# Kernel optimization log

Measured on AMD Instinct MI355X. Metric: run time of the kernel, lower is better.

## Reference

```python
import jax, jax.numpy as jnp
import numpy as np

B, C_IN, T_IN = 128, 128, 2500
C_OUT, K, STRIDE, PAD = 64, 27, 4, 13  # T_out = 625
BN_EPS = 1e-5
SURROGATE_ALPHA = 4.0


def binarize_weight(w):
    """1-bit (XNOR-Net style) weight quantization with straight-through estimator.
    w: (O, I, K). Per-output-channel scale = mean |w|."""
    alpha = jnp.mean(jnp.abs(w), axis=(1, 2), keepdims=True)
    wq = jnp.sign(w) * alpha
    return w + jax.lax.stop_gradient(wq - w)


def spike(x):
    """Heaviside spike with sigmoid surrogate gradient (STE)."""
    hard = (x > 0).astype(x.dtype)
    soft = jax.nn.sigmoid(SURROGATE_ALPHA * x)
    return soft + jax.lax.stop_gradient(hard - soft)


def setup_inputs() -> dict:
    key = jax.random.key(0)
    ks = jax.random.split(key, 8)
    scale_conv = 1.0 / np.sqrt(C_IN * K)
    scale_lin = 1.0 / np.sqrt(C_OUT)
    return {
        "x": jax.random.normal(ks[0], (B, C_IN, T_IN), dtype=jnp.float32),
        "conv_w": jax.random.normal(ks[1], (C_OUT, C_IN, K), dtype=jnp.float32) * scale_conv,
        "conv_b": jnp.zeros((C_OUT,), dtype=jnp.float32),
        "bn_gamma": jnp.ones((C_OUT,), dtype=jnp.float32),
        "bn_beta": jnp.zeros((C_OUT,), dtype=jnp.float32),
        "bn_mean": jax.random.normal(ks[2], (C_OUT,), dtype=jnp.float32) * 0.1,
        "bn_var": jax.random.uniform(ks[3], (C_OUT,), dtype=jnp.float32, minval=0.5, maxval=1.5),
        "wq": jax.random.normal(ks[4], (C_OUT, C_OUT), dtype=jnp.float32) * scale_lin,
        "wk": jax.random.normal(ks[5], (C_OUT, C_OUT), dtype=jnp.float32) * scale_lin,
        "wv": jax.random.normal(ks[6], (C_OUT, C_OUT), dtype=jnp.float32) * scale_lin,
        "wo": jax.random.normal(ks[7], (C_OUT, C_OUT), dtype=jnp.float32) * scale_lin,
    }


def reference(x, conv_w, conv_b, bn_gamma, bn_beta, bn_mean, bn_var, wq, wk, wv, wo):
    # --- 1-bit quantized conv1d, stride 4 ---
    w_bin = binarize_weight(conv_w)
    y = jax.lax.conv_general_dilated(
        x, w_bin, window_strides=(STRIDE,), padding=[(PAD, PAD)],
        dimension_numbers=("NCH", "OIH", "NCH"))
    y = y + conv_b[None, :, None]  # (B, C_OUT, 625)

    # --- BatchNorm1d (inference stats) + ELU ---
    inv = jax.lax.rsqrt(bn_var + BN_EPS)
    y = (y - bn_mean[None, :, None]) * (inv * bn_gamma)[None, :, None] + bn_beta[None, :, None]
    y = jax.nn.elu(y)

    # --- Global spiking attention (single head) ---
    s = spike(y)                                   # (B, C, T) binary spikes
    q = jnp.einsum("oc,bct->bot", wq, s)           # (B, C, T)
    k = jnp.einsum("oc,bct->bot", wk, s)
    v = jnp.einsum("oc,bct->bot", wv, y)
    scores = jnp.einsum("bct,bcs->bts", q, k) / jnp.sqrt(jnp.asarray(C_OUT, y.dtype))
    attn = jax.nn.softmax(scores, axis=-1)         # (B, T, T)
    ctx = jnp.einsum("bts,bcs->bct", attn, v)      # (B, C, T)
    out = y + jnp.einsum("oc,bct->bot", wo, ctx)   # residual
    return out
```

## Files before the change

kernel.cpp:

```cpp
#include <hip/hip_runtime.h>
#include <math.h>

#define B_    128
#define CIN   128
#define TIN   2500
#define COUT  64
#define KW    27
#define TOUT  625
#define TPAD  640
#define CTT   32
#define GROWS 152

typedef __bf16 bf16x8 __attribute__((ext_vector_type(8)));
typedef float  f32x4  __attribute__((ext_vector_type(4)));

__device__ __forceinline__ unsigned short f32_to_bf16_rne(float v) {
    unsigned u = __float_as_uint(v);
    u += 0x7FFFu + ((u >> 16) & 1u);
    return (unsigned short)(u >> 16);
}

__device__ __forceinline__ f32x4 mfma_bf16(bf16x8 a, bf16x8 b, f32x4 c) {
    return __builtin_amdgcn_mfma_f32_16x16x32_bf16(a, b, c, 0, 0, 0);
}

__device__ __forceinline__ bf16x8 expand_sgn(unsigned b) {
    union { unsigned u[4]; bf16x8 v; } r;
#pragma unroll
    for (int j = 0; j < 4; j++) {
        unsigned lo = (b >> (2 * j)) & 1u;
        unsigned hi = (b >> (2 * j + 1)) & 1u;
        r.u[j] = 0x3F803F80u | (lo << 15) | (hi << 31);
    }
    return r.v;
}

__global__ void binarize_kernel(const float* __restrict__ w,
                                unsigned* __restrict__ sgn2,
                                float* __restrict__ alpha_out) {
    int o = blockIdx.x, tid = threadIdx.x;
    __shared__ float red[256];
    const float* wo_ = w + (size_t)o * (CIN * KW);
    float s = 0.f;
    for (int idx = tid; idx < CIN * KW; idx += 256) s += fabsf(wo_[idx]);
    red[tid] = s;
    __syncthreads();
    for (int st = 128; st > 0; st >>= 1) {
        if (tid < st) red[tid] += red[tid + st];
        __syncthreads();
    }
    if (tid == 0) alpha_out[o] = red[0] / (float)(CIN * KW);

    for (int t = tid; t < KW * 4; t += 256) {
        int kk = t >> 2, kg = t & 3;
        unsigned u = 0;
#pragma unroll
        for (int cs = 0; cs < 4; cs++) {
#pragma unroll
            for (int j = 0; j < 8; j++) {
                int c = cs * 32 + kg * 8 + j;
                float v = wo_[c * KW + kk];
                unsigned bit = (v > 0.f) ? 0u : 1u;
                u |= bit << (cs * 8 + j);
            }
        }
        sgn2[(kk * 4 + kg) * 64 + o] = u;
    }
}

__global__ void transpose_w_kernel(const float* __restrict__ wq, const float* __restrict__ wk,
                                   const float* __restrict__ wv, const float* __restrict__ wo,
                                   const float* __restrict__ conv_b, const float* __restrict__ gamma_,
                                   const float* __restrict__ beta_, const float* __restrict__ mean_,
                                   const float* __restrict__ var_, const float* __restrict__ alpha_,
                                   float* __restrict__ dstT,
                                   unsigned short* __restrict__ wo_h, unsigned short* __restrict__ wo_l,
                                   float* __restrict__ scA, float* __restrict__ scB) {
    if (blockIdx.x < 3) {
        const float* srcs[3] = {wq, wk, wv};
        const float* src = srcs[blockIdx.x];
        float* dst = dstT + (size_t)blockIdx.x * 4096;
        for (int idx = threadIdx.x; idx < 4096; idx += 256) {
            int o = idx >> 6, c = idx & 63;
            dst[c * 64 + o] = src[idx];
        }
    } else if (blockIdx.x == 3) {
        for (int idx = threadIdx.x; idx < 4096; idx += 256) {
            float v = wo[idx];
            unsigned short h = f32_to_bf16_rne(v);
            float hf = __uint_as_float((unsigned)h << 16);
            wo_h[idx] = h;
            wo_l[idx] = f32_to_bf16_rne(v - hf);
        }
    } else {
        int o = threadIdx.x;
        if (o < 64) {
            float inv = rsqrtf(var_[o] + 1e-5f);
            float G = gamma_[o] * inv;
            scA[o] = alpha_[o] * G;
            scB[o] = (conv_b[o] - mean_[o]) * G + beta_[o];
        }
    }
}

__global__ __launch_bounds__(256, 4) void conv_kernel(
    const float* __restrict__ x, const unsigned* __restrict__ sgn2,
    const float* __restrict__ scA, const float* __restrict__ scB,
    float* __restrict__ y_out)
{
    __shared__ __align__(16) unsigned short xhi[GROWS * 128];

    int b = blockIdx.y;
    int t0 = blockIdx.x * CTT;
    int tid = threadIdx.x;

    const float* xb = x + (size_t)b * CIN * TIN;
    int gbase = 4 * t0 - 13;
    for (int task = tid; task < 16 * GROWS; task += 256) {
        int c8 = task / GROWS, gl = task - c8 * GROWS;
        int g = gbase + gl;
        bool valid = (gl < 151) && ((unsigned)g < (unsigned)TIN);
        float vs[8];
#pragma unroll
        for (int j = 0; j < 8; j++)
            vs[j] = valid ? xb[(size_t)(c8 * 8 + j) * TIN + g] : 0.f;
        union { unsigned u[4]; uint4 q; } H;
#pragma unroll
        for (int j = 0; j < 4; j++) {
            unsigned short h0 = f32_to_bf16_rne(vs[2 * j]);
            unsigned short h1 = f32_to_bf16_rne(vs[2 * j + 1]);
            H.u[j] = (unsigned)h0 | ((unsigned)h1 << 16);
        }
        int c8p = c8 ^ ((gl >> 2) & 15);
        *(uint4*)(xhi + gl * 128 + c8p * 8) = H.q;
    }
    __syncthreads();

    int wave = tid >> 6, lane = tid & 63;
    int o0 = wave * 16;
    int n = lane & 15, kg = lane >> 4;

    f32x4 acc0 = {0.f, 0.f, 0.f, 0.f};
    f32x4 acc1 = {0.f, 0.f, 0.f, 0.f};

    const unsigned* sgb = sgn2 + (size_t)kg * 64 + o0 + n;
    unsigned sa = sgb[0];

#pragma unroll 1
    for (int kk = 0; kk < KW; ++kk) {
        unsigned na = 0;
        if (kk < KW - 1) na = sgb[(kk + 1) * 256];
        int gl = 4 * n + kk;
        int rot = (gl >> 2) & 15;
        const unsigned short* xr0 = xhi + gl * 128;
        const unsigned short* xr1 = xr0 + 8192;
#pragma unroll
        for (int cs = 0; cs < 4; ++cs) {
            int c8p = (cs * 4 + kg) ^ rot;
            bf16x8 b0 = *(const bf16x8*)(xr0 + c8p * 8);
            bf16x8 b1 = *(const bf16x8*)(xr1 + c8p * 8);
            bf16x8 a = expand_sgn((sa >> (8 * cs)) & 0xFFu);
            acc0 = mfma_bf16(a, b0, acc0);
            acc1 = mfma_bf16(a, b1, acc1);
        }
        sa = na;
    }

    int quad = lane >> 4, col = lane & 15;
#pragma unroll
    for (int tt = 0; tt < 2; ++tt) {
        int t_g = t0 + tt * 16 + col;
        if (t_g < TOUT) {
            f32x4 a = tt ? acc1 : acc0;
#pragma unroll
            for (int r = 0; r < 4; ++r) {
                int o = o0 + quad * 4 + r;
                float s = a[r] * scA[o] + scB[o];
                float yv = s > 0.f ? s : expm1f(s);
                y_out[((size_t)b * COUT + o) * TOUT + t_g] = yv;
            }
        }
    }
}

__global__ __launch_bounds__(256, 2) void proj_kernel(
    const float* __restrict__ y, const float* __restrict__ wqT,
    const float* __restrict__ wkT, const float* __restrict__ wvT,
    unsigned short* __restrict__ q_h, unsigned short* __restrict__ k_h,
    unsigned short* __restrict__ vT_h)
{
    __shared__ float y_sh[64 * 132];
    int b = blockIdx.y, t0 = blockIdx.x * 128, tid = threadIdx.x;

    const float* yb = y + (size_t)b * COUT * TOUT;
    for (int i = tid; i < 64 * 128; i += 256) {
        int c = i >> 7, tt = i & 127;
        int t = t0 + tt;
        y_sh[c * 132 + tt] = (t < TOUT) ? yb[c * TOUT + t] : 0.f;
    }
    __syncthreads();

    int oo = tid & 63, tq = tid >> 6;
    float q[32], k[32], v[32];
#pragma unroll
    for (int j = 0; j < 32; j++) { q[j] = 0.f; k[j] = 0.f; v[j] = 0.f; }

#pragma unroll 1
    for (int c = 0; c < 64; ++c) {
        float wq = wqT[c * 64 + oo];
        float wk = wkT[c * 64 + oo];
        float wv = wvT[c * 64 + oo];
        const float* yr = &y_sh[c * 132 + tq * 32];
#pragma unroll
        for (int j = 0; j < 32; ++j) {
            float yv = yr[j];
            float sp = yv > 0.f ? 1.f : 0.f;
            q[j] += wq * sp; k[j] += wk * sp; v[j] += wv * yv;
        }
    }

    int tbase = t0 + tq * 32;
#pragma unroll
    for (int j = 0; j < 32; ++j) {
        size_t off = ((size_t)b * TPAD + tbase + j) * 64 + oo;
        q_h[off] = f32_to_bf16_rne(q[j]);
        k_h[off] = f32_to_bf16_rne(k[j]);
    }
    union { unsigned short u[32]; uint4 q4[4]; } V;
#pragma unroll
    for (int j = 0; j < 32; ++j) V.u[j] = f32_to_bf16_rne(v[j]);
    unsigned short* vp = vT_h + ((size_t)b * 64 + oo) * TPAD + tbase;
#pragma unroll
    for (int i = 0; i < 4; i++) ((uint4*)vp)[i] = V.q4[i];
}

__global__ __launch_bounds__(256, 3) void attn_kernel(
    const unsigned short* __restrict__ q_h, const unsigned short* __restrict__ k_h,
    const unsigned short* __restrict__ vT_h, const float* __restrict__ y,
    const unsigned short* __restrict__ wo_h, const unsigned short* __restrict__ wo_l,
    float* __restrict__ out)
{
    __shared__ float sc_sh[16 * 648];
    __shared__ float ctx_sh[64 * 17];
    __shared__ float red_sh[256];
    __shared__ float rden[16];

    int b = blockIdx.y, t0 = blockIdx.x * 16, tid = threadIdx.x;
    int wave = tid >> 6, lane = tid & 63;
    int quad = lane >> 4, nlo = lane & 15;

    const unsigned short* qb = q_h + ((size_t)b * TPAD + t0 + nlo) * 64 + quad * 8;
    bf16x8 qa0 = *(const bf16x8*)(qb);
    bf16x8 qa1 = *(const bf16x8*)(qb + 32);
    const unsigned short* kbase = k_h + (size_t)b * TPAD * 64 + quad * 8;
#pragma unroll 5
    for (int nt = 0; nt < 10; ++nt) {
        int s = (wave * 10 + nt) * 16 + nlo;
        const unsigned short* krow = kbase + (size_t)s * 64;
        bf16x8 kb0 = *(const bf16x8*)(krow);
        bf16x8 kb1 = *(const bf16x8*)(krow + 32);
        f32x4 acc = {0.f, 0.f, 0.f, 0.f};
        acc = mfma_bf16(qa0, kb0, acc);
        acc = mfma_bf16(qa1, kb1, acc);
#pragma unroll
        for (int r = 0; r < 4; ++r)
            sc_sh[(quad * 4 + r) * 648 + s] = acc[r] * 0.125f;
    }
    __syncthreads();

    int ti1 = tid >> 4, sg = tid & 15;
    float mx = -3.0e38f;
    for (int s = sg; s < TOUT; s += 16) mx = fmaxf(mx, sc_sh[ti1 * 648 + s]);
    red_sh[tid] = mx;
    __syncthreads();
    float rowm = red_sh[ti1 * 16];
#pragma unroll
    for (int l = 1; l < 16; l++) rowm = fmaxf(rowm, red_sh[ti1 * 16 + l]);
    __syncthreads();
    float sum = 0.f;
    for (int s = sg; s < TOUT; s += 16) {
        float e = __expf(sc_sh[ti1 * 648 + s] - rowm);
        sc_sh[ti1 * 648 + s] = e;
        sum += e;
    }
    red_sh[tid] = sum;
    __syncthreads();
    if (tid < 16) {
        float tot = 0.f;
#pragma unroll
        for (int l = 0; l < 16; l++) tot += red_sh[tid * 16 + l];
        rden[tid] = 1.f / tot;
    }
    __syncthreads();

    const unsigned short* vb = vT_h + ((size_t)b * 64 + wave * 16 + nlo) * TPAD;
    f32x4 cacc = {0.f, 0.f, 0.f, 0.f};
#pragma unroll 4
    for (int ks = 0; ks < 20; ++ks) {
        const float* pr = &sc_sh[nlo * 648 + ks * 32 + quad * 8];
        union { unsigned short u[8]; bf16x8 v; } P;
#pragma unroll
        for (int j = 0; j < 8; ++j) P.u[j] = f32_to_bf16_rne(pr[j]);
        bf16x8 v8 = *(const bf16x8*)(vb + ks * 32 + quad * 8);
        cacc = mfma_bf16(P.v, v8, cacc);
    }
#pragma unroll
    for (int r = 0; r < 4; ++r)
        ctx_sh[(wave * 16 + nlo) * 17 + quad * 4 + r] = cacc[r] * rden[quad * 4 + r];
    __syncthreads();

    const unsigned short* woh = wo_h + (size_t)(wave * 16 + nlo) * 64 + quad * 8;
    const unsigned short* wol = wo_l + (size_t)(wave * 16 + nlo) * 64 + quad * 8;
    f32x4 oacc = {0.f, 0.f, 0.f, 0.f};
#pragma unroll
    for (int ks = 0; ks < 2; ++ks) {
        union { unsigned short u[8]; bf16x8 v; } Bc;
#pragma unroll
        for (int j = 0; j < 8; ++j)
            Bc.u[j] = f32_to_bf16_rne(ctx_sh[(ks * 32 + quad * 8 + j) * 17 + nlo]);
        bf16x8 ah = *(const bf16x8*)(woh + ks * 32);
        bf16x8 al = *(const bf16x8*)(wol + ks * 32);
        oacc = mfma_bf16(ah, Bc.v, oacc);
        oacc = mfma_bf16(al, Bc.v, oacc);
    }
    int t_g = t0 + nlo;
    if (t_g < TOUT) {
#pragma unroll
        for (int r = 0; r < 4; ++r) {
            int o = wave * 16 + quad * 4 + r;
            size_t off = ((size_t)b * COUT + o) * TOUT + t_g;
            out[off] = y[off] + oacc[r];
        }
    }
}

extern "C" void kernel_launch(void* const* d_in, const int* in_sizes, int n_in,
                              void* d_out, int out_size, void* d_ws, size_t ws_size,
                              hipStream_t stream) {
    const float* x        = (const float*)d_in[0];
    const float* conv_w   = (const float*)d_in[1];
    const float* conv_b   = (const float*)d_in[2];
    const float* bn_gamma = (const float*)d_in[3];
    const float* bn_beta  = (const float*)d_in[4];
    const float* bn_mean  = (const float*)d_in[5];
    const float* bn_var   = (const float*)d_in[6];
    const float* wq       = (const float*)d_in[7];
    const float* wk       = (const float*)d_in[8];
    const float* wv       = (const float*)d_in[9];
    const float* wo       = (const float*)d_in[10];
    float* out = (float*)d_out;
    float* ws  = (float*)d_ws;

    unsigned* sgn2        = (unsigned*)ws;
    float* alpha          = ws + 110592;
    float* scA            = ws + 110656;
    float* scB            = ws + 110720;
    float* wT4            = ws + 110848;
    unsigned short* wo_h  = (unsigned short*)(ws + 123136);
    unsigned short* wo_l  = (unsigned short*)(ws + 125184);
    float* yb             = ws + 131072;
    unsigned short* q_h   = (unsigned short*)(ws + 5251072);
    unsigned short* k_h   = (unsigned short*)(ws + 7872512);
    unsigned short* vT_h  = (unsigned short*)(ws + 10493952);

    hipLaunchKernelGGL(binarize_kernel, dim3(64), dim3(256), 0, stream, conv_w, sgn2, alpha);
    hipLaunchKernelGGL(transpose_w_kernel, dim3(5), dim3(256), 0, stream,
                       wq, wk, wv, wo, conv_b, bn_gamma, bn_beta, bn_mean, bn_var, alpha,
                       wT4, wo_h, wo_l, scA, scB);
    hipLaunchKernelGGL(conv_kernel, dim3(20, 128), dim3(256), 0, stream,
                       x, sgn2, scA, scB, yb);
    hipLaunchKernelGGL(proj_kernel, dim3(5, 128), dim3(256), 0, stream,
                       yb, wT4, wT4 + 4096, wT4 + 8192, q_h, k_h, vT_h);
    hipLaunchKernelGGL(attn_kernel, dim3(40, 128), dim3(256), 0, stream,
                       q_h, k_h, vT_h, yb, wo_h, wo_l, out);
}
```

Before: 497.8 us.

## Double attention block width and halve proj tile with shared-memory weights

The attention kernel now runs 512 threads per block. The score, softmax and P·V stages are split across 8 waves, and the two K-halves of the context are reduced through shared memory before the output projection, which only 4 waves perform. The projection kernel uses 64-wide time tiles, which doubles the grid and cuts per-thread accumulators from 96 to 48. It also stages Wq/Wk/Wv into shared memory and reads y as float4. The aim is more parallelism and occupancy on the 128x40 attention grid and lower register pressure in the projection. The cost is more synchronisation, idle waves during the output projection, and more shared memory per block.

```diff
diff --git a/kernel.cpp b/kernel.cpp
--- a/kernel.cpp
+++ b/kernel.cpp
@@ -189,60 +189,73 @@
     unsigned short* __restrict__ q_h, unsigned short* __restrict__ k_h,
     unsigned short* __restrict__ vT_h)
 {
-    __shared__ float y_sh[64 * 132];
-    int b = blockIdx.y, t0 = blockIdx.x * 128, tid = threadIdx.x;
-
+    __shared__ float w_sh[3 * 4096];
+    __shared__ __align__(16) float y_sh[64 * 72];
+    int b = blockIdx.y, t0 = blockIdx.x * 64, tid = threadIdx.x;
+
+    for (int i = tid; i < 4096; i += 256) {
+        w_sh[i]         = wqT[i];
+        w_sh[4096 + i]  = wkT[i];
+        w_sh[8192 + i]  = wvT[i];
+    }
     const float* yb = y + (size_t)b * COUT * TOUT;
-    for (int i = tid; i < 64 * 128; i += 256) {
-        int c = i >> 7, tt = i & 127;
+    for (int i = tid; i < 64 * 64; i += 256) {
+        int c = i >> 6, tt = i & 63;
         int t = t0 + tt;
-        y_sh[c * 132 + tt] = (t < TOUT) ? yb[c * TOUT + t] : 0.f;
+        y_sh[c * 72 + tt] = (t < TOUT) ? yb[c * TOUT + t] : 0.f;
     }
     __syncthreads();
 
     int oo = tid & 63, tq = tid >> 6;
-    float q[32], k[32], v[32];
-#pragma unroll
-    for (int j = 0; j < 32; j++) { q[j] = 0.f; k[j] = 0.f; v[j] = 0.f; }
+    float q[16], k[16], v[16];
+#pragma unroll
+    for (int j = 0; j < 16; j++) { q[j] = 0.f; k[j] = 0.f; v[j] = 0.f; }
 
 #pragma unroll 1
     for (int c = 0; c < 64; ++c) {
-        float wq = wqT[c * 64 + oo];
-        float wk = wkT[c * 64 + oo];
-        float wv = wvT[c * 64 + oo];
-        const float* yr = &y_sh[c * 132 + tq * 32];
-#pragma unroll
-        for (int j = 0; j < 32; ++j) {
-            float yv = yr[j];
-            float sp = yv > 0.f ? 1.f : 0.f;
-            q[j] += wq * sp; k[j] += wk * sp; v[j] += wv * yv;
-        }
-    }
-
-    int tbase = t0 + tq * 32;
-#pragma unroll
-    for (int j = 0; j < 32; ++j) {
+        float wq = w_sh[c * 64 + oo];
+        float wk = w_sh[4096 + c * 64 + oo];
+        float wv = w_sh[8192 + c * 64 + oo];
+        const float* yr = &y_sh[c * 72 + tq * 16];
+#pragma unroll
+        for (int j4 = 0; j4 < 4; ++j4) {
+            float4 y4 = *(const float4*)(yr + 4 * j4);
+            float ys[4] = {y4.x, y4.y, y4.z, y4.w};
+#pragma unroll
+            for (int j = 0; j < 4; ++j) {
+                float yv = ys[j];
+                float sp = yv > 0.f ? 1.f : 0.f;
+                q[4 * j4 + j] += wq * sp;
+                k[4 * j4 + j] += wk * sp;
+                v[4 * j4 + j] += wv * yv;
+            }
+        }
+    }
+
+    int tbase = t0 + tq * 16;
+#pragma unroll
+    for (int j = 0; j < 16; ++j) {
         size_t off = ((size_t)b * TPAD + tbase + j) * 64 + oo;
         q_h[off] = f32_to_bf16_rne(q[j]);
         k_h[off] = f32_to_bf16_rne(k[j]);
     }
-    union { unsigned short u[32]; uint4 q4[4]; } V;
-#pragma unroll
-    for (int j = 0; j < 32; ++j) V.u[j] = f32_to_bf16_rne(v[j]);
+    union { unsigned short u[16]; uint4 q4[2]; } V;
+#pragma unroll
+    for (int j = 0; j < 16; ++j) V.u[j] = f32_to_bf16_rne(v[j]);
     unsigned short* vp = vT_h + ((size_t)b * 64 + oo) * TPAD + tbase;
-#pragma unroll
-    for (int i = 0; i < 4; i++) ((uint4*)vp)[i] = V.q4[i];
-}
-
-__global__ __launch_bounds__(256, 3) void attn_kernel(
+    ((uint4*)vp)[0] = V.q4[0];
+    ((uint4*)vp)[1] = V.q4[1];
+}
+
+__global__ __launch_bounds__(512, 3) void attn_kernel(
     const unsigned short* __restrict__ q_h, const unsigned short* __restrict__ k_h,
     const unsigned short* __restrict__ vT_h, const float* __restrict__ y,
     const unsigned short* __restrict__ wo_h, const unsigned short* __restrict__ wo_l,
     float* __restrict__ out)
 {
     __shared__ float sc_sh[16 * 648];
-    __shared__ float ctx_sh[64 * 17];
-    __shared__ float red_sh[256];
+    __shared__ float ctx_sh[2 * 64 * 17];
+    __shared__ float red_sh[512];
     __shared__ float rden[16];
 
     int b = blockIdx.y, t0 = blockIdx.x * 16, tid = threadIdx.x;
@@ -254,8 +267,8 @@
     bf16x8 qa1 = *(const bf16x8*)(qb + 32);
     const unsigned short* kbase = k_h + (size_t)b * TPAD * 64 + quad * 8;
 #pragma unroll 5
-    for (int nt = 0; nt < 10; ++nt) {
-        int s = (wave * 10 + nt) * 16 + nlo;
+    for (int nt = 0; nt < 5; ++nt) {
+        int s = wave * 80 + nt * 16 + nlo;
         const unsigned short* krow = kbase + (size_t)s * 64;
         bf16x8 kb0 = *(const bf16x8*)(krow);
         bf16x8 kb1 = *(const bf16x8*)(krow + 32);
@@ -268,17 +281,17 @@
     }
     __syncthreads();
 
-    int ti1 = tid >> 4, sg = tid & 15;
+    int ti1 = tid >> 5, sg = tid & 31;
     float mx = -3.0e38f;
-    for (int s = sg; s < TOUT; s += 16) mx = fmaxf(mx, sc_sh[ti1 * 648 + s]);
+    for (int s = sg; s < TOUT; s += 32) mx = fmaxf(mx, sc_sh[ti1 * 648 + s]);
     red_sh[tid] = mx;
     __syncthreads();
-    float rowm = red_sh[ti1 * 16];
-#pragma unroll
-    for (int l = 1; l < 16; l++) rowm = fmaxf(rowm, red_sh[ti1 * 16 + l]);
+    float rowm = red_sh[ti1 * 32];
+#pragma unroll
+    for (int l = 1; l < 32; l++) rowm = fmaxf(rowm, red_sh[ti1 * 32 + l]);
     __syncthreads();
     float sum = 0.f;
-    for (int s = sg; s < TOUT; s += 16) {
+    for (int s = sg; s < TOUT; s += 32) {
         float e = __expf(sc_sh[ti1 * 648 + s] - rowm);
         sc_sh[ti1 * 648 + s] = e;
         sum += e;
@@ -288,15 +301,18 @@
     if (tid < 16) {
         float tot = 0.f;
 #pragma unroll
-        for (int l = 0; l < 16; l++) tot += red_sh[tid * 16 + l];
+        for (int l = 0; l < 32; l++) tot += red_sh[tid * 32 + l];
         rden[tid] = 1.f / tot;
     }
     __syncthreads();
 
-    const unsigned short* vb = vT_h + ((size_t)b * 64 + wave * 16 + nlo) * TPAD;
+    int cw = (wave & 3) * 16, kh = wave >> 2;
+    const unsigned short* vb = vT_h + ((size_t)b * 64 + cw + nlo) * TPAD;
     f32x4 cacc = {0.f, 0.f, 0.f, 0.f};
-#pragma unroll 4
-    for (int ks = 0; ks < 20; ++ks) {
+    int ks0 = kh * 10;
+#pragma unroll 5
+    for (int i = 0; i < 10; ++i) {
+        int ks = ks0 + i;
         const float* pr = &sc_sh[nlo * 648 + ks * 32 + quad * 8];
         union { unsigned short u[8]; bf16x8 v; } P;
 #pragma unroll
@@ -306,30 +322,35 @@
     }
 #pragma unroll
     for (int r = 0; r < 4; ++r)
-        ctx_sh[(wave * 16 + nlo) * 17 + quad * 4 + r] = cacc[r] * rden[quad * 4 + r];
-    __syncthreads();
-
-    const unsigned short* woh = wo_h + (size_t)(wave * 16 + nlo) * 64 + quad * 8;
-    const unsigned short* wol = wo_l + (size_t)(wave * 16 + nlo) * 64 + quad * 8;
-    f32x4 oacc = {0.f, 0.f, 0.f, 0.f};
-#pragma unroll
-    for (int ks = 0; ks < 2; ++ks) {
-        union { unsigned short u[8]; bf16x8 v; } Bc;
-#pragma unroll
-        for (int j = 0; j < 8; ++j)
-            Bc.u[j] = f32_to_bf16_rne(ctx_sh[(ks * 32 + quad * 8 + j) * 17 + nlo]);
-        bf16x8 ah = *(const bf16x8*)(woh + ks * 32);
-        bf16x8 al = *(const bf16x8*)(wol + ks * 32);
-        oacc = mfma_bf16(ah, Bc.v, oacc);
-        oacc = mfma_bf16(al, Bc.v, oacc);
-    }
-    int t_g = t0 + nlo;
-    if (t_g < TOUT) {
-#pragma unroll
-        for (int r = 0; r < 4; ++r) {
-            int o = wave * 16 + quad * 4 + r;
-            size_t off = ((size_t)b * COUT + o) * TOUT + t_g;
-            out[off] = y[off] + oacc[r];
+        ctx_sh[kh * 1088 + (cw + nlo) * 17 + quad * 4 + r] = cacc[r] * rden[quad * 4 + r];
+    __syncthreads();
+
+    if (wave < 4) {
+        const unsigned short* woh = wo_h + (size_t)(wave * 16 + nlo) * 64 + quad * 8;
+        const unsigned short* wol = wo_l + (size_t)(wave * 16 + nlo) * 64 + quad * 8;
+        f32x4 oacc = {0.f, 0.f, 0.f, 0.f};
+#pragma unroll
+        for (int ks = 0; ks < 2; ++ks) {
+            union { unsigned short u[8]; bf16x8 v; } Bc;
+#pragma unroll
+            for (int j = 0; j < 8; ++j) {
+                int c = ks * 32 + quad * 8 + j;
+                float cv = ctx_sh[c * 17 + nlo] + ctx_sh[1088 + c * 17 + nlo];
+                Bc.u[j] = f32_to_bf16_rne(cv);
+            }
+            bf16x8 ah = *(const bf16x8*)(woh + ks * 32);
+            bf16x8 al = *(const bf16x8*)(wol + ks * 32);
+            oacc = mfma_bf16(ah, Bc.v, oacc);
+            oacc = mfma_bf16(al, Bc.v, oacc);
+        }
+        int t_g = t0 + nlo;
+        if (t_g < TOUT) {
+#pragma unroll
+            for (int r = 0; r < 4; ++r) {
+                int o = wave * 16 + quad * 4 + r;
+                size_t off = ((size_t)b * COUT + o) * TOUT + t_g;
+                out[off] = y[off] + oacc[r];
+            }
         }
     }
 }
@@ -369,8 +390,8 @@
                        wT4, wo_h, wo_l, scA, scB);
     hipLaunchKernelGGL(conv_kernel, dim3(20, 128), dim3(256), 0, stream,
                        x, sgn2, scA, scB, yb);
-    hipLaunchKernelGGL(proj_kernel, dim3(5, 128), dim3(256), 0, stream,
+    hipLaunchKernelGGL(proj_kernel, dim3(10, 128), dim3(256), 0, stream,
                        yb, wT4, wT4 + 4096, wT4 + 8192, q_h, k_h, vT_h);
-    hipLaunchKernelGGL(attn_kernel, dim3(40, 128), dim3(256), 0, stream,
+    hipLaunchKernelGGL(attn_kernel, dim3(40, 128), dim3(512), 0, stream,
                        q_h, k_h, vT_h, yb, wo_h, wo_l, out);
 }
```

New measurement: 494.7 us. About the same (-0.6%).
